# Optimization experiments

Hardware: AMD Instinct MI355X
Metric: run time of the kernel (lower is better)

The kernel has to match this reference:

```python
import jax, jax.numpy as jnp
import numpy as np
from jax import lax

KERNEL_EPS = 1e-4   # eps in softmax_kernel
ATTN_EPS = 1e-6     # eps in causal_linear_attention
CHUNK = 64          # chunk length for the causal scan


def softmax_kernel(data, projection_matrix, is_query):
    # data: [b,h,n,d], projection_matrix: [r,d]
    d = data.shape[-1]
    r = projection_matrix.shape[0]
    data_normalizer = d ** -0.25
    ratio = r ** -0.5
    data_dash = jnp.einsum('bhnd,rd->bhnr', data_normalizer * data, projection_matrix)
    diag_data = (jnp.sum(data ** 2, axis=-1) * 0.5 * data_normalizer ** 2)[..., None]  # [b,h,n,1]
    if is_query:
        stab = jnp.max(data_dash, axis=-1, keepdims=True)
    else:
        stab = jnp.max(data_dash)
    return ratio * (jnp.exp(data_dash - diag_data - stab) + KERNEL_EPS)


def causal_linear_attention(qp, kp, v, chunk=CHUNK, eps=ATTN_EPS):
    # qp,kp: [b,h,n,r] feature maps; v: [b,h,n,e]
    b, h, n, r = qp.shape
    e = v.shape[-1]
    nc = n // chunk
    # -> [nc, b, h, chunk, *] for lax.scan over chunks
    qs = jnp.moveaxis(qp.reshape(b, h, nc, chunk, r), 2, 0)
    ks = jnp.moveaxis(kp.reshape(b, h, nc, chunk, r), 2, 0)
    vs = jnp.moveaxis(v.reshape(b, h, nc, chunk, e), 2, 0)

    def step(carry, xs):
        k_last, ctx_last = carry  # [b,h,r], [b,h,r,e]
        qch, kch, vch = xs        # [b,h,c,r], [b,h,c,r], [b,h,c,e]
        k_cum = k_last[:, :, None, :] + jnp.cumsum(kch, axis=2)              # [b,h,c,r]
        D_inv = 1.0 / jnp.einsum('bhcr,bhcr->bhc', qch, k_cum + eps)         # [b,h,c]
        ctx = jnp.einsum('bhcr,bhce->bhcre', kch, vch)                       # [b,h,c,r,e]
        ctx_cum = ctx_last[:, :, None] + jnp.cumsum(ctx, axis=2)             # [b,h,c,r,e]
        out = jnp.einsum('bhcre,bhcr,bhc->bhce', ctx_cum, qch, D_inv)        # [b,h,c,e]
        return (k_cum[:, :, -1], ctx_cum[:, :, -1]), out

    init = (jnp.zeros((b, h, r), qp.dtype), jnp.zeros((b, h, r, e), qp.dtype))
    _, outs = lax.scan(step, init, (qs, ks, vs))  # outs: [nc,b,h,c,e]
    return jnp.moveaxis(outs, 0, 2).reshape(b, h, n, e)


def setup_inputs() -> dict:
    key = jax.random.key(0)
    kq, kk, kv, kp = jax.random.split(key, 4)
    b, h, n, d, r = 2, 8, 4096, 64, 256
    q = jax.random.normal(kq, (b, h, n, d), dtype=jnp.float32)
    k = jax.random.normal(kk, (b, h, n, d), dtype=jnp.float32)
    v = jax.random.normal(kv, (b, h, n, d), dtype=jnp.float32)
    projection_matrix = jax.random.normal(kp, (r, d), dtype=jnp.float32)
    return {"q": q, "k": k, "v": v, "projection_matrix": projection_matrix}


def reference(q, k, v, projection_matrix):
    qp = softmax_kernel(q, projection_matrix, is_query=True)
    kp = softmax_kernel(k, projection_matrix, is_query=False)
    return causal_linear_attention(qp, kp, v)
```

## Files before the change

kernel.cpp:

```cpp
#include <hip/hip_runtime.h>


typedef unsigned short ushort_t;
typedef __attribute__((ext_vector_type(8))) short bf16x8;
typedef __attribute__((ext_vector_type(4))) float f32x4;

#define KEPS 1e-4f
#define AEPS 1e-6f
#define NORMIZER 0.35355339059327373f
#define RATIO 0.0625f

__device__ __forceinline__ ushort_t bf16r(float f) {
  unsigned u = __float_as_uint(f);
  return (ushort_t)((u + 0x7fffu + ((u >> 16) & 1u)) >> 16);
}
__device__ __forceinline__ float ubf(ushort_t h) {
  return __uint_as_float((unsigned)h << 16);
}

__global__ __launch_bounds__(256) void pconv_kernel(
    const float* __restrict__ P, ushort_t* __restrict__ Phi,
    ushort_t* __restrict__ Plo)
{
  int idx = blockIdx.x * 1024 + threadIdx.x;
  #pragma unroll
  for (int p = 0; p < 4; ++p) {
    int i = idx + p * 256;
    float x = P[i];
    ushort_t h = bf16r(x);
    Phi[i] = h;
    Plo[i] = bf16r(x - ubf(h));
  }
}

__device__ __forceinline__ void stage_ptile(const ushort_t* __restrict__ gt,
                                            ushort_t* lds0, int tid) {
  int wv = tid >> 6, lane = tid & 63;
  #pragma unroll
  for (int i = 0; i < 2; ++i) {
    int D = i * 256 + wv * 64 + lane;
    int row = D >> 3, c3 = D & 7;
    int sc = (row << 3) | (c3 ^ (row & 7));
    __builtin_amdgcn_global_load_lds(
        (const __attribute__((address_space(1))) void*)(gt + sc * 8),
        (__attribute__((address_space(3))) void*)(lds0 + (i * 256 + wv * 64) * 8),
        16, 0, 0);
  }
}

__global__ __launch_bounds__(256, 4) void feat_mfma(
    const float* __restrict__ Q, const float* __restrict__ K,
    const ushort_t* __restrict__ Phi, const ushort_t* __restrict__ Plo,
    ushort_t* __restrict__ qp, ushort_t* __restrict__ E,
    float* __restrict__ bmax)
{
  __shared__ union {
    struct {
      ushort_t Xhi[64 * 72];
      ushort_t Xlo[64 * 72];
      ushort_t Pt[2][4096];
    } s;
    ushort_t outb[64 * 268];
  } u;
  __shared__ float diagS[64];
  __shared__ float redm[4];

  int bid = blockIdx.x, tid = threadIdx.x;
  bool isK = bid >= 1024;
  const float* X = isK ? K : Q;
  size_t rowbase = (size_t)(isK ? bid - 1024 : bid) * 64;

  stage_ptile(Phi, &u.s.Pt[0][0], tid);

  #pragma unroll
  for (int p = 0; p < 4; ++p) {
    int idx = tid + p * 256;
    int row = idx >> 4, c4 = idx & 15;
    float4 x = *(const float4*)&X[(rowbase + row) * 64 + c4 * 4];
    ushort4 h, l;
    h.x = bf16r(x.x); l.x = bf16r(x.x - ubf(h.x));
    h.y = bf16r(x.y); l.y = bf16r(x.y - ubf(h.y));
    h.z = bf16r(x.z); l.z = bf16r(x.z - ubf(h.z));
    h.w = bf16r(x.w); l.w = bf16r(x.w - ubf(h.w));
    *(ushort4*)&u.s.Xhi[row * 72 + c4 * 4] = h;
    *(ushort4*)&u.s.Xlo[row * 72 + c4 * 4] = l;
    float ss = x.x * x.x + x.y * x.y + x.z * x.z + x.w * x.w;
    ss += __shfl_xor(ss, 1, 64); ss += __shfl_xor(ss, 2, 64);
    ss += __shfl_xor(ss, 4, 64); ss += __shfl_xor(ss, 8, 64);
    if ((tid & 15) == 0) diagS[row] = 0.0625f * ss;
  }
  __syncthreads();

  int lane = tid & 63, wv = tid >> 6;
  int n15 = lane & 15, quad = lane >> 4;

  bf16x8 ah[2], al[2];
  #pragma unroll
  for (int ks = 0; ks < 2; ++ks) {
    int off = (16 * wv + n15) * 72 + quad * 8 + 32 * ks;
    ah[ks] = *(const bf16x8*)&u.s.Xhi[off];
    al[ks] = *(const bf16x8*)&u.s.Xlo[off];
  }

  f32x4 acc[16];
  #pragma unroll
  for (int tc = 0; tc < 16; ++tc) acc[tc] = f32x4{0.f, 0.f, 0.f, 0.f};

  int buf = 0;
  #pragma unroll
  for (int t = 0; t < 8; ++t) {
    int q4 = t >> 1;
    bool isLo = t & 1;
    if (t) {
      asm volatile("s_waitcnt vmcnt(0)" ::: "memory");
      __builtin_amdgcn_s_barrier();
    }
    if (t < 7) {
      int tn = t + 1;
      const ushort_t* gt = ((tn & 1) ? Plo : Phi) + (size_t)(tn >> 1) * 4096;
      stage_ptile(gt, &u.s.Pt[buf ^ 1][0], tid);
    }
    #pragma unroll
    for (int tcl = 0; tcl < 4; ++tcl) {
      f32x4 a = acc[q4 * 4 + tcl];
      #pragma unroll
      for (int ks = 0; ks < 2; ++ks) {
        int jr = 16 * tcl + n15;
        int rc = (quad + 4 * ks) ^ (n15 & 7);
        bf16x8 b = *(const bf16x8*)&u.s.Pt[buf][jr * 64 + rc * 8];
        a = __builtin_amdgcn_mfma_f32_16x16x32_bf16(ah[ks], b, a, 0, 0, 0);
        if (!isLo)
          a = __builtin_amdgcn_mfma_f32_16x16x32_bf16(al[ks], b, a, 0, 0, 0);
      }
      acc[q4 * 4 + tcl] = a;
    }
    buf ^= 1;
  }

  float dg[4];
  #pragma unroll
  for (int r = 0; r < 4; ++r) dg[r] = diagS[16 * wv + quad * 4 + r];

  float sub[4];
  if (!isK) {
    #pragma unroll
    for (int r = 0; r < 4; ++r) {
      float mx = -3.0e38f;
      #pragma unroll
      for (int tc = 0; tc < 16; ++tc) mx = fmaxf(mx, acc[tc][r]);
      #pragma unroll
      for (int s = 1; s < 16; s <<= 1) mx = fmaxf(mx, __shfl_xor(mx, s, 64));
      sub[r] = dg[r] + NORMIZER * mx;
    }
  } else {
    float bm = -3.0e38f;
    #pragma unroll
    for (int tc = 0; tc < 16; ++tc)
      #pragma unroll
      for (int r = 0; r < 4; ++r) bm = fmaxf(bm, acc[tc][r]);
    #pragma unroll
    for (int s = 1; s < 64; s <<= 1) bm = fmaxf(bm, __shfl_xor(bm, s, 64));
    if (lane == 0) redm[wv] = bm;
    #pragma unroll
    for (int r = 0; r < 4; ++r) sub[r] = dg[r];
  }

  __syncthreads();
  ushort_t* dst = (isK ? E : qp) + rowbase * 256;
  #pragma unroll
  for (int tc = 0; tc < 16; ++tc) {
    #pragma unroll
    for (int r = 0; r < 4; ++r) {
      int row = 16 * wv + quad * 4 + r;
      float ex = __expf(NORMIZER * acc[tc][r] - sub[r]);
      float val = isK ? ex : RATIO * (ex + KEPS);
      u.outb[row * 268 + 16 * tc + n15] = bf16r(val);
    }
  }
  __syncthreads();
  #pragma unroll
  for (int p = 0; p < 8; ++p) {
    int g = (tid + p * 256) * 8;
    int row = g >> 8, c0 = g & 255;
    bf16x8 v0 = *(const bf16x8*)&u.outb[row * 268 + c0];
    *(bf16x8*)&dst[row * 256 + c0] = v0;
  }

  if (isK && tid == 0) {
    float m4 = fmaxf(fmaxf(redm[0], redm[1]), fmaxf(redm[2], redm[3]));
    bmax[bid - 1024] = NORMIZER * m4;
  }
}

__global__ __launch_bounds__(256) void kmax_reduce(
    const float* __restrict__ bmax, float* __restrict__ kmax)
{
  __shared__ float red[4];
  int tid = threadIdx.x;
  float m = fmaxf(fmaxf(bmax[tid], bmax[tid + 256]),
                  fmaxf(bmax[tid + 512], bmax[tid + 768]));
  #pragma unroll
  for (int s = 1; s < 64; s <<= 1) m = fmaxf(m, __shfl_xor(m, s, 64));
  if ((tid & 63) == 0) red[tid >> 6] = m;
  __syncthreads();
  if (tid == 0)
    *kmax = fmaxf(fmaxf(red[0], red[1]), fmaxf(red[2], red[3]));
}

__global__ __launch_bounds__(256) void chunksum_mfma(
    const ushort_t* __restrict__ E, const float* __restrict__ V,
    ushort_t* __restrict__ SE, float* __restrict__ zE, float* __restrict__ SV)
{
  __shared__ ushort_t Et[256 * 72];
  __shared__ ushort_t Vt[64 * 72];
  __shared__ float red2[256];

  int bc = blockIdx.x, tid = threadIdx.x;
  size_t ebase = (size_t)bc * 16384;

  #pragma unroll
  for (int p = 0; p < 8; ++p) {
    int g = (tid + p * 256) * 8;
    int pos = g >> 8, j0 = g & 255;
    bf16x8 ev = *(const bf16x8*)&E[ebase + g];
    #pragma unroll
    for (int jj = 0; jj < 8; ++jj) {
      int j = j0 + jj;
      int pr = (pos + 8 * ((j >> 3) & 7)) & 63;
      Et[j * 72 + pr] = (ushort_t)ev[jj];
    }
  }
  float vsum = 0.f;
  #pragma unroll
  for (int p = 0; p < 16; ++p) {
    int g = tid + p * 256;
    int pos = g >> 6, e = g & 63;
    float x = V[(size_t)bc * 4096 + g];
    vsum += x;
    int pr = (pos + 8 * ((e >> 3) & 7)) & 63;
    Vt[e * 72 + pr] = bf16r(x);
  }
  red2[tid] = vsum;
  __syncthreads();
  if (tid < 64)
    SV[(size_t)bc * 64 + tid] =
        red2[tid] + red2[64 + tid] + red2[128 + tid] + red2[192 + tid];

  {
    float s = 0.f;
    #pragma unroll
    for (int m8 = 0; m8 < 8; ++m8) {
      bf16x8 r8 = *(const bf16x8*)&Et[tid * 72 + m8 * 8];
      #pragma unroll
      for (int x = 0; x < 8; ++x) s += ubf((ushort_t)r8[x]);
    }
    zE[(size_t)bc * 256 + tid] = s;
  }

  int lane = tid & 63, wv = tid >> 6;
  int n15 = lane & 15, quad = lane >> 4;

  bf16x8 aV[2];
  {
    int e = 16 * wv + n15;
    int rot = 8 * ((e >> 3) & 7);
    #pragma unroll
    for (int ks = 0; ks < 2; ++ks) {
      int pr = (quad * 8 + 32 * ks + rot) & 63;
      aV[ks] = *(const bf16x8*)&Vt[e * 72 + pr];
    }
  }

  f32x4 acc[16];
  #pragma unroll
  for (int tc = 0; tc < 16; ++tc) {
    int j = 16 * tc + n15;
    int rot = 8 * ((j >> 3) & 7);
    f32x4 a = {0.f, 0.f, 0.f, 0.f};
    #pragma unroll
    for (int ks = 0; ks < 2; ++ks) {
      int pr = (quad * 8 + 32 * ks + rot) & 63;
      bf16x8 b = *(const bf16x8*)&Et[j * 72 + pr];
      a = __builtin_amdgcn_mfma_f32_16x16x32_bf16(aV[ks], b, a, 0, 0, 0);
    }
    acc[tc] = a;
  }
  __syncthreads();

  ushort_t* outS = Et;
  #pragma unroll
  for (int tc = 0; tc < 16; ++tc)
    #pragma unroll
    for (int r = 0; r < 4; ++r) {
      int e = 16 * wv + quad * 4 + r;
      outS[e * 264 + 16 * tc + n15] = bf16r(acc[tc][r]);
    }
  __syncthreads();
  #pragma unroll
  for (int p = 0; p < 8; ++p) {
    int g = (tid + p * 256) * 8;
    int e = g >> 8, j0 = g & 255;
    bf16x8 vv = *(const bf16x8*)&outS[e * 264 + j0];
    *(bf16x8*)&SE[ebase + g] = vv;
  }
}

__global__ __launch_bounds__(256) void prefix_kernel(
    ushort_t* __restrict__ S, float* __restrict__ zE,
    const float* __restrict__ SV, const float* __restrict__ kmax)
{
  int b = blockIdx.x;
  float m = *kmax;
  float c1 = RATIO * __expf(-m);
  const float c0 = RATIO * KEPS;
  if (b < 1024) {
    int flat = b * 256 + threadIdx.x;
    int bh = flat >> 14;
    int idx = flat & 16383;
    int e = idx >> 8;
    size_t base = (size_t)bh * 1048576 + idx;
    const float* svp = SV + (size_t)bh * 4096 + e;
    float runE = 0.f, runV = 0.f;
    for (int cc = 0; cc < 64; cc += 8) {
      ushort_t t[8]; float sv[8];
      #pragma unroll
      for (int u2 = 0; u2 < 8; ++u2) {
        t[u2] = S[base + (size_t)(cc + u2) * 16384];
        sv[u2] = svp[(size_t)(cc + u2) * 64];
      }
      #pragma unroll
      for (int u2 = 0; u2 < 8; ++u2) {
        S[base + (size_t)(cc + u2) * 16384] = bf16r(c1 * runE + c0 * runV);
        runE += ubf(t[u2]);
        runV += sv[u2];
      }
    }
  } else {
    int bh = b - 1024;
    int j = threadIdx.x;
    size_t base = (size_t)bh * 16384 + j;
    float run = 0.f;
    for (int cc = 0; cc < 64; cc += 8) {
      float t[8];
      #pragma unroll
      for (int u2 = 0; u2 < 8; ++u2)
        t[u2] = zE[base + (size_t)(cc + u2) * 256];
      #pragma unroll
      for (int u2 = 0; u2 < 8; ++u2) {
        zE[base + (size_t)(cc + u2) * 256] = run;
        run += c1 * t[u2] + 64.0f * c0;
      }
    }
  }
}

__device__ __forceinline__ void stage_tile(const ushort_t* __restrict__ gt,
                                           ushort_t* lds0, int tid, int wv) {
  #pragma unroll
  for (int i = 0; i < 2; ++i) {
    int D = i * 256 + tid;
    int row = D >> 5, cl = D & 31;
    int sc = (row << 5) | (cl ^ (row & 7));
    __builtin_amdgcn_global_load_lds(
        (const __attribute__((address_space(1))) void*)(gt + sc * 8),
        (__attribute__((address_space(3))) void*)(lds0 + (i * 256 + wv * 64) * 8),
        16, 0, 0);
  }
}

__global__ __launch_bounds__(256) void fused_mfma(
    const ushort_t* __restrict__ qp, const ushort_t* __restrict__ E,
    const float* __restrict__ kmax, const float* __restrict__ Z,
    const ushort_t* __restrict__ S, const float* __restrict__ V,
    float* __restrict__ out)
{
  __shared__ ushort_t As[64 * 72];
  __shared__ ushort_t Vt[64 * 72];
  __shared__ ushort_t Bst[2][4096];
  __shared__ float zv[256];
  __shared__ float qsumS[64];
  __shared__ float dqS[64];

  int bc = blockIdx.x, tid = threadIdx.x;
  int lane = tid & 63, wv = tid >> 6;
  int n15 = lane & 15, quad = lane >> 4;
  float m = *kmax;
  float c1 = RATIO * __expf(-m);
  const float c0 = RATIO * KEPS;
  size_t base = (size_t)bc * 16384;

  zv[tid] = Z[(size_t)bc * 256 + tid] + AEPS;
  #pragma unroll
  for (int p = 0; p < 16; ++p) {
    int idx = tid + p * 256;
    int t = idx >> 6, e = idx & 63;
    Vt[e * 72 + t] = bf16r(V[(size_t)bc * 4096 + idx]);
  }
  __syncthreads();

  stage_tile(E + base, &Bst[0][0], tid, wv);

  bf16x8 aQ[8];
  #pragma unroll
  for (int ks = 0; ks < 8; ++ks)
    aQ[ks] = *(const bf16x8*)&qp[base + (size_t)(16 * wv + n15) * 256 + quad * 8 + 32 * ks];

  float qsum = 0.f, dq = 0.f;
  #pragma unroll
  for (int ks = 0; ks < 8; ++ks)
    #pragma unroll
    for (int j = 0; j < 8; ++j) {
      float qv = ubf((ushort_t)aQ[ks][j]);
      qsum += qv;
      dq += qv * zv[quad * 8 + 32 * ks + j];
    }
  qsum += __shfl_xor(qsum, 16, 64); qsum += __shfl_xor(qsum, 32, 64);
  dq   += __shfl_xor(dq, 16, 64);   dq   += __shfl_xor(dq, 32, 64);
  if (quad == 0) { qsumS[16 * wv + n15] = qsum; dqS[16 * wv + n15] = dq; }

  float rs[4] = {0.f, 0.f, 0.f, 0.f};
  float dinv[4] = {0.f, 0.f, 0.f, 0.f};

  #pragma unroll
  for (int t = 0; t < 8; ++t) {
    asm volatile("s_waitcnt vmcnt(0)" ::: "memory");
    __builtin_amdgcn_s_barrier();
    if (t < 7) {
      const ushort_t* gt = (t < 3) ? (E + base + (size_t)(t + 1) * 4096)
                                   : (S + base + (size_t)(t - 3) * 4096);
      stage_tile(gt, &Bst[(t + 1) & 1][0], tid, wv);
    }

    bf16x8 bf[8];
    #pragma unroll
    for (int ks = 0; ks < 8; ++ks) {
      int rc = (4 * ks + quad) ^ (n15 & 7);
      bf[ks] = *(const bf16x8*)&Bst[t & 1][(n15 * 32 + rc) * 8];
    }
    f32x4 g = {0.f, 0.f, 0.f, 0.f};
    #pragma unroll
    for (int ks = 0; ks < 8; ++ks)
      g = __builtin_amdgcn_mfma_f32_16x16x32_bf16(aQ[ks], bf[ks], g, 0, 0, 0);

    if (t < 4) {
      int tc = t;
      #pragma unroll
      for (int r = 0; r < 4; ++r) {
        int i = 16 * wv + quad * 4 + r;
        int tt = 16 * tc + n15;
        float val = (tt <= i) ? (c1 * g[r] + c0 * qsumS[i]) : 0.f;
        As[i * 72 + tt] = bf16r(val);
        rs[r] += val;
      }
      if (t == 3) {
        #pragma unroll
        for (int r = 0; r < 4; ++r) {
          float v2 = rs[r];
          #pragma unroll
          for (int s = 1; s < 16; s <<= 1) v2 += __shfl_xor(v2, s, 64);
          int i = 16 * wv + quad * 4 + r;
          dinv[r] = 1.f / (dqS[i] + v2);
        }
      }
    } else {
      int ec = t - 4;
      f32x4 o = g;
      #pragma unroll
      for (int ks = 0; ks < 2; ++ks) {
        bf16x8 a2 = *(const bf16x8*)&As[(16 * wv + n15) * 72 + quad * 8 + 32 * ks];
        bf16x8 b2 = *(const bf16x8*)&Vt[(16 * ec + n15) * 72 + quad * 8 + 32 * ks];
        o = __builtin_amdgcn_mfma_f32_16x16x32_bf16(a2, b2, o, 0, 0, 0);
      }
      #pragma unroll
      for (int r = 0; r < 4; ++r) {
        int i = 16 * wv + quad * 4 + r;
        out[(size_t)bc * 4096 + (size_t)i * 64 + 16 * ec + n15] = o[r] * dinv[r];
      }
    }
  }
}

extern "C" void kernel_launch(void* const* d_in, const int* in_sizes, int n_in,
                              void* d_out, int out_size, void* d_ws, size_t ws_size,
                              hipStream_t stream)
{
  const float* q = (const float*)d_in[0];
  const float* k = (const float*)d_in[1];
  const float* v = (const float*)d_in[2];
  const float* P = (const float*)d_in[3];
  float* out = (float*)d_out;

  ushort_t* qp  = (ushort_t*)d_ws;
  ushort_t* E   = qp + 16777216;
  ushort_t* S   = E + 16777216;
  float*    zE  = (float*)(S + 16777216);
  float*    SV  = zE + 262144;
  ushort_t* Phi = (ushort_t*)(SV + 65536);
  ushort_t* Plo = Phi + 16384;
  float*    bmax = (float*)(Plo + 16384);
  float*    kmax = bmax + 1024;

  pconv_kernel<<<16, 256, 0, stream>>>(P, Phi, Plo);
  feat_mfma<<<2048, 256, 0, stream>>>(q, k, Phi, Plo, qp, E, bmax);
  kmax_reduce<<<1, 256, 0, stream>>>(bmax, kmax);
  chunksum_mfma<<<1024, 256, 0, stream>>>(E, v, S, zE, SV);
  prefix_kernel<<<1040, 256, 0, stream>>>(S, zE, SV, kmax);
  fused_mfma<<<1024, 256, 0, stream>>>(qp, E, kmax, zE, S, v, out);
}
```

Before: 166.8 us.

## Fuse chunk-sum MFMA into feature kernel's K blocks, drop chunksum launch

```diff
diff --git a/kernel.cpp b/kernel.cpp
--- a/kernel.cpp
+++ b/kernel.cpp
@@ -48,11 +48,14 @@
   }
 }
 
-__global__ __launch_bounds__(256, 4) void feat_mfma(
+__global__ __launch_bounds__(256, 3) void feat_mfma(
     const float* __restrict__ Q, const float* __restrict__ K,
+    const float* __restrict__ V,
     const ushort_t* __restrict__ Phi, const ushort_t* __restrict__ Plo,
     ushort_t* __restrict__ qp, ushort_t* __restrict__ E,
-    float* __restrict__ bmax)
+    float* __restrict__ bmax,
+    ushort_t* __restrict__ SE, float* __restrict__ zE,
+    float* __restrict__ SV)
 {
   __shared__ union {
     struct {
@@ -61,16 +64,27 @@
       ushort_t Pt[2][4096];
     } s;
     ushort_t outb[64 * 268];
+    ushort_t Et[256 * 72];
   } u;
+  __shared__ ushort_t Vt[64 * 72];
+  __shared__ float red2[256];
   __shared__ float diagS[64];
   __shared__ float redm[4];
 
   int bid = blockIdx.x, tid = threadIdx.x;
   bool isK = bid >= 1024;
+  int bc = bid - 1024;
   const float* X = isK ? K : Q;
-  size_t rowbase = (size_t)(isK ? bid - 1024 : bid) * 64;
+  size_t rowbase = (size_t)(isK ? bc : bid) * 64;
 
   stage_ptile(Phi, &u.s.Pt[0][0], tid);
+
+  float vv[16];
+  if (isK) {
+    #pragma unroll
+    for (int p = 0; p < 16; ++p)
+      vv[p] = V[rowbase * 64 + tid + p * 256];
+  }
 
   #pragma unroll
   for (int p = 0; p < 4; ++p) {
@@ -165,6 +179,7 @@
     for (int r = 0; r < 4; ++r) sub[r] = dg[r];
   }
 
+  unsigned hp[16][2];
   __syncthreads();
   ushort_t* dst = (isK ? E : qp) + rowbase * 256;
   #pragma unroll
@@ -174,7 +189,10 @@
       int row = 16 * wv + quad * 4 + r;
       float ex = __expf(NORMIZER * acc[tc][r] - sub[r]);
       float val = isK ? ex : RATIO * (ex + KEPS);
-      u.outb[row * 268 + 16 * tc + n15] = bf16r(val);
+      ushort_t h = bf16r(val);
+      u.outb[row * 268 + 16 * tc + n15] = h;
+      if (r & 1) hp[tc][r >> 1] |= ((unsigned)h << 16);
+      else       hp[tc][r >> 1] = (unsigned)h;
     }
   }
   __syncthreads();
@@ -188,7 +206,96 @@
 
   if (isK && tid == 0) {
     float m4 = fmaxf(fmaxf(redm[0], redm[1]), fmaxf(redm[2], redm[3]));
-    bmax[bid - 1024] = NORMIZER * m4;
+    bmax[bc] = NORMIZER * m4;
+  }
+
+  if (!isK) return;
+
+  __syncthreads();
+
+  float vsum = 0.f;
+  #pragma unroll
+  for (int p = 0; p < 16; ++p) {
+    int g = tid + p * 256;
+    int pos = g >> 6, e = g & 63;
+    float x = vv[p];
+    vsum += x;
+    int pr = (pos + 8 * ((e >> 3) & 7)) & 63;
+    Vt[e * 72 + pr] = bf16r(x);
+  }
+  red2[tid] = vsum;
+
+  #pragma unroll
+  for (int tc = 0; tc < 16; ++tc) {
+    int j = 16 * tc + n15;
+    int rot = 8 * ((j >> 3) & 7);
+    int pw = (16 * wv + quad * 4 + rot) & 63;
+    ushort4 w4;
+    w4.x = (ushort_t)(hp[tc][0] & 0xffffu);
+    w4.y = (ushort_t)(hp[tc][0] >> 16);
+    w4.z = (ushort_t)(hp[tc][1] & 0xffffu);
+    w4.w = (ushort_t)(hp[tc][1] >> 16);
+    *(ushort4*)&u.Et[j * 72 + pw] = w4;
+  }
+  __syncthreads();
+
+  if (tid < 64)
+    SV[(size_t)bc * 64 + tid] =
+        red2[tid] + red2[64 + tid] + red2[128 + tid] + red2[192 + tid];
+
+  {
+    float s = 0.f;
+    #pragma unroll
+    for (int m8 = 0; m8 < 8; ++m8) {
+      bf16x8 r8 = *(const bf16x8*)&u.Et[tid * 72 + m8 * 8];
+      #pragma unroll
+      for (int x = 0; x < 8; ++x) s += ubf((ushort_t)r8[x]);
+    }
+    zE[(size_t)bc * 256 + tid] = s;
+  }
+
+  bf16x8 aV[2];
+  {
+    int e = 16 * wv + n15;
+    int rot = 8 * ((e >> 3) & 7);
+    #pragma unroll
+    for (int ks = 0; ks < 2; ++ks) {
+      int pr = (quad * 8 + 32 * ks + rot) & 63;
+      aV[ks] = *(const bf16x8*)&Vt[e * 72 + pr];
+    }
+  }
+
+  f32x4 acc2[16];
+  #pragma unroll
+  for (int tc = 0; tc < 16; ++tc) {
+    int j = 16 * tc + n15;
+    int rot = 8 * ((j >> 3) & 7);
+    f32x4 a = {0.f, 0.f, 0.f, 0.f};
+    #pragma unroll
+    for (int ks = 0; ks < 2; ++ks) {
+      int pr = (quad * 8 + 32 * ks + rot) & 63;
+      bf16x8 b = *(const bf16x8*)&u.Et[j * 72 + pr];
+      a = __builtin_amdgcn_mfma_f32_16x16x32_bf16(aV[ks], b, a, 0, 0, 0);
+    }
+    acc2[tc] = a;
+  }
+  __syncthreads();
+
+  #pragma unroll
+  for (int tc = 0; tc < 16; ++tc)
+    #pragma unroll
+    for (int r = 0; r < 4; ++r) {
+      int e = 16 * wv + quad * 4 + r;
+      u.outb[e * 268 + 16 * tc + n15] = bf16r(acc2[tc][r]);
+    }
+  __syncthreads();
+  ushort_t* sdst = SE + rowbase * 256;
+  #pragma unroll
+  for (int p = 0; p < 8; ++p) {
+    int g = (tid + p * 256) * 8;
+    int e = g >> 8, j0 = g & 255;
+    bf16x8 v0 = *(const bf16x8*)&u.outb[e * 268 + j0];
+    *(bf16x8*)&sdst[e * 256 + j0] = v0;
   }
 }
 
@@ -205,104 +312,6 @@
   __syncthreads();
   if (tid == 0)
     *kmax = fmaxf(fmaxf(red[0], red[1]), fmaxf(red[2], red[3]));
-}
-
-__global__ __launch_bounds__(256) void chunksum_mfma(
-    const ushort_t* __restrict__ E, const float* __restrict__ V,
-    ushort_t* __restrict__ SE, float* __restrict__ zE, float* __restrict__ SV)
-{
-  __shared__ ushort_t Et[256 * 72];
-  __shared__ ushort_t Vt[64 * 72];
-  __shared__ float red2[256];
-
-  int bc = blockIdx.x, tid = threadIdx.x;
-  size_t ebase = (size_t)bc * 16384;
-
-  #pragma unroll
-  for (int p = 0; p < 8; ++p) {
-    int g = (tid + p * 256) * 8;
-    int pos = g >> 8, j0 = g & 255;
-    bf16x8 ev = *(const bf16x8*)&E[ebase + g];
-    #pragma unroll
-    for (int jj = 0; jj < 8; ++jj) {
-      int j = j0 + jj;
-      int pr = (pos + 8 * ((j >> 3) & 7)) & 63;
-      Et[j * 72 + pr] = (ushort_t)ev[jj];
-    }
-  }
-  float vsum = 0.f;
-  #pragma unroll
-  for (int p = 0; p < 16; ++p) {
-    int g = tid + p * 256;
-    int pos = g >> 6, e = g & 63;
-    float x = V[(size_t)bc * 4096 + g];
-    vsum += x;
-    int pr = (pos + 8 * ((e >> 3) & 7)) & 63;
-    Vt[e * 72 + pr] = bf16r(x);
-  }
-  red2[tid] = vsum;
-  __syncthreads();
-  if (tid < 64)
-    SV[(size_t)bc * 64 + tid] =
-        red2[tid] + red2[64 + tid] + red2[128 + tid] + red2[192 + tid];
-
-  {
-    float s = 0.f;
-    #pragma unroll
-    for (int m8 = 0; m8 < 8; ++m8) {
-      bf16x8 r8 = *(const bf16x8*)&Et[tid * 72 + m8 * 8];
-      #pragma unroll
-      for (int x = 0; x < 8; ++x) s += ubf((ushort_t)r8[x]);
-    }
-    zE[(size_t)bc * 256 + tid] = s;
-  }
-
-  int lane = tid & 63, wv = tid >> 6;
-  int n15 = lane & 15, quad = lane >> 4;
-
-  bf16x8 aV[2];
-  {
-    int e = 16 * wv + n15;
-    int rot = 8 * ((e >> 3) & 7);
-    #pragma unroll
-    for (int ks = 0; ks < 2; ++ks) {
-      int pr = (quad * 8 + 32 * ks + rot) & 63;
-      aV[ks] = *(const bf16x8*)&Vt[e * 72 + pr];
-    }
-  }
-
-  f32x4 acc[16];
-  #pragma unroll
-  for (int tc = 0; tc < 16; ++tc) {
-    int j = 16 * tc + n15;
-    int rot = 8 * ((j >> 3) & 7);
-    f32x4 a = {0.f, 0.f, 0.f, 0.f};
-    #pragma unroll
-    for (int ks = 0; ks < 2; ++ks) {
-      int pr = (quad * 8 + 32 * ks + rot) & 63;
-      bf16x8 b = *(const bf16x8*)&Et[j * 72 + pr];
-      a = __builtin_amdgcn_mfma_f32_16x16x32_bf16(aV[ks], b, a, 0, 0, 0);
-    }
-    acc[tc] = a;
-  }
-  __syncthreads();
-
-  ushort_t* outS = Et;
-  #pragma unroll
-  for (int tc = 0; tc < 16; ++tc)
-    #pragma unroll
-    for (int r = 0; r < 4; ++r) {
-      int e = 16 * wv + quad * 4 + r;
-      outS[e * 264 + 16 * tc + n15] = bf16r(acc[tc][r]);
-    }
-  __syncthreads();
-  #pragma unroll
-  for (int p = 0; p < 8; ++p) {
-    int g = (tid + p * 256) * 8;
-    int e = g >> 8, j0 = g & 255;
-    bf16x8 vv = *(const bf16x8*)&outS[e * 264 + j0];
-    *(bf16x8*)&SE[ebase + g] = vv;
-  }
 }
 
 __global__ __launch_bounds__(256) void prefix_kernel(
@@ -501,9 +510,9 @@
   float*    kmax = bmax + 1024;
 
   pconv_kernel<<<16, 256, 0, stream>>>(P, Phi, Plo);
-  feat_mfma<<<2048, 256, 0, stream>>>(q, k, Phi, Plo, qp, E, bmax);
+  feat_mfma<<<2048, 256, 0, stream>>>(q, k, v, Phi, Plo, qp, E, bmax,
+                                      S, zE, SV);
   kmax_reduce<<<1, 256, 0, stream>>>(bmax, kmax);
-  chunksum_mfma<<<1024, 256, 0, stream>>>(E, v, S, zE, SV);
   prefix_kernel<<<1040, 256, 0, stream>>>(S, zE, SV, kmax);
   fused_mfma<<<1024, 256, 0, stream>>>(qp, E, kmax, zE, S, v, out);
 }
```

After: 166.8 us. No clear change (+0.0%).
